# Optimization experiments

Measured on AMD Instinct MI355X. Metric: run time of the kernel, lower is better.

Reference implementation:

```python
import jax, jax.numpy as jnp
import numpy as np

NUM_HEADS = 16


def _local_attn(q, k, v, bias, nq, nk):
    """Blocked local attention, faithful to rearrange_to_dense_trunk semantics.
    q,k,v: [B,H,N,D]; bias: [B,Hb,N,N] (Hb broadcasts against H).
    Trunk i (queries [i*nq,(i+1)*nq)) attends keys at original indices
    [i*nq - pad_left, i*nq - pad_left + nk); out-of-range keys/values/bias are
    zero-padded (the module pads with zeros, no -inf key masking).
    Assumes N % nq == 0 (q_pad_length == 0, so the query mask loop is a no-op).
    """
    B, H, N, D = q.shape
    T = N // nq                      # n_trunks
    pad_left = (nk - nq) // 2
    Lp = (T - 1) * nq + nk           # padded key length so every window is full
    pad_right = Lp - pad_left - N
    k_p = jnp.pad(k, ((0, 0), (0, 0), (pad_left, pad_right), (0, 0)))
    v_p = jnp.pad(v, ((0, 0), (0, 0), (pad_left, pad_right), (0, 0)))
    b_p = jnp.pad(bias, ((0, 0), (0, 0), (0, 0), (pad_left, pad_right)))
    # window gather indices: [T, nk]
    kidx = jnp.arange(T)[:, None] * nq + jnp.arange(nk)[None, :]
    k_t = k_p[:, :, kidx, :]         # [B,H,T,nk,D]
    v_t = v_p[:, :, kidx, :]         # [B,H,T,nk,D]
    Bb, Hb = bias.shape[0], bias.shape[1]
    b_r = b_p.reshape(Bb, Hb, T, nq, Lp)
    b_t = jnp.take_along_axis(b_r, kidx[None, None, :, None, :], axis=-1)  # [Bb,Hb,T,nq,nk]
    q_t = q.reshape(B, H, T, nq, D)
    scores = jnp.einsum('bhtqd,bhtkd->bhtqk', q_t, k_t) + b_t
    w = jax.nn.softmax(scores, axis=-1)
    o = jnp.einsum('bhtqk,bhtkd->bhtqd', w, v_t)
    return o.reshape(B, H, N, D)


def setup_inputs() -> dict:
    key = jax.random.key(0)
    ks = jax.random.split(key, 8)
    B, N, C = 1, 4096, 256
    H, D = NUM_HEADS, 64
    HD = H * D
    q_x = jax.random.normal(ks[0], (B, N, C), dtype=jnp.float32)
    kv_x = jax.random.normal(ks[1], (B, N, C), dtype=jnp.float32)
    attn_bias = jax.random.normal(ks[2], (B, 1, N, N), dtype=jnp.float32) * 0.1
    Wq = jax.random.normal(ks[3], (C, HD), dtype=jnp.float32) / np.sqrt(C).astype(np.float32)
    Wk = jax.random.normal(ks[4], (C, HD), dtype=jnp.float32) / np.sqrt(C).astype(np.float32)
    Wv = jax.random.normal(ks[5], (C, HD), dtype=jnp.float32) / np.sqrt(C).astype(np.float32)
    Wg = jax.random.normal(ks[6], (C, HD), dtype=jnp.float32) / np.sqrt(C).astype(np.float32)
    Wo = jax.random.normal(ks[7], (HD, C), dtype=jnp.float32) / np.sqrt(HD).astype(np.float32)
    return {"q_x": q_x, "kv_x": kv_x, "attn_bias": attn_bias,
            "Wq": Wq, "Wk": Wk, "Wv": Wv, "Wg": Wg, "Wo": Wo,
            "n_queries": 64, "n_keys": 256}


def reference(q_x, kv_x, attn_bias, Wq, Wk, Wv, Wg, Wo, n_queries, n_keys):
    B, N, C = q_x.shape
    H = NUM_HEADS
    D = Wq.shape[-1] // H
    def split_heads(x):
        return x.reshape(B, N, H, D).transpose(0, 2, 1, 3)  # [B,H,N,D]
    q = split_heads(q_x @ Wq) / jnp.sqrt(jnp.float32(D))
    k = split_heads(kv_x @ Wk)
    v = split_heads(kv_x @ Wv)
    o = _local_attn(q, k, v, attn_bias, n_queries, n_keys)
    o = o.transpose(0, 2, 1, 3).reshape(B, N, H * D)
    g = jax.nn.sigmoid(q_x @ Wg)  # gating head
    return (o * g) @ Wo
```

## Files before the change

kernel.cpp:

```cpp
#include <hip/hip_runtime.h>

#define N_ 4096
#define C_ 256
#define H_ 16
#define D_ 64
#define HD_ 1024

typedef __attribute__((ext_vector_type(8))) __bf16 bf16x8;
typedef __attribute__((ext_vector_type(4))) __bf16 bf16x4;
typedef __attribute__((ext_vector_type(8))) _Float16 f16x8;
typedef __attribute__((ext_vector_type(4))) float f32x4;

__device__ __forceinline__ void gload16(const void* g, void* l) {
    __builtin_amdgcn_global_load_lds(
        (const __attribute__((address_space(1))) unsigned int*)g,
        (__attribute__((address_space(3))) unsigned int*)l, 16, 0, 0);
}

struct bf2 { __bf16 h, l; };
__device__ __forceinline__ bf2 split_bf16(float v) {
    bf2 r;
    r.h = (__bf16)v;
    r.l = (__bf16)(v - (float)r.h);
    return r;
}

__global__ __launch_bounds__(256) void convert_kernel(
    const float* __restrict__ q_x, const float* __restrict__ kv_x,
    const float* __restrict__ Wq, const float* __restrict__ Wk,
    const float* __restrict__ Wv, const float* __restrict__ Wg,
    const float* __restrict__ Wo,
    __bf16* __restrict__ Xh, __bf16* __restrict__ Xl,
    __bf16* __restrict__ WTh, __bf16* __restrict__ WTl,
    __bf16* __restrict__ WoTh, __bf16* __restrict__ WoTl)
{
    __shared__ float ts[64][65];
    const int b = blockIdx.x;
    const int tid = threadIdx.x;

    if (b < 512) {
        const int seg = b >> 8;
        const float* src = seg ? kv_x : q_x;
        __bf16* dh = Xh + (size_t)seg * 1048576;
        __bf16* dl = Xl + (size_t)seg * 1048576;
        const int base = (b & 255) * 4096 + tid * 16;
#pragma unroll
        for (int q = 0; q < 4; ++q) {
            float4 v = *(const float4*)&src[base + q * 4];
            bf16x4 hv, lv;
            bf2 s0 = split_bf16(v.x); hv[0] = s0.h; lv[0] = s0.l;
            bf2 s1 = split_bf16(v.y); hv[1] = s1.h; lv[1] = s1.l;
            bf2 s2 = split_bf16(v.z); hv[2] = s2.h; lv[2] = s2.l;
            bf2 s3 = split_bf16(v.w); hv[3] = s3.h; lv[3] = s3.l;
            *(bf16x4*)&dh[base + q * 4] = hv;
            *(bf16x4*)&dl[base + q * 4] = lv;
        }
        return;
    }

    const float* src;
    __bf16 *dh, *dl;
    int srcC, dstC, r0, c0;
    if (b < 768) {
        const int widx = (b - 512) >> 6;
        const int tile = (b - 512) & 63;
        src = (widx == 0) ? Wq : (widx == 1) ? Wk : (widx == 2) ? Wv : Wg;
        dh = WTh + (size_t)widx * 262144;
        dl = WTl + (size_t)widx * 262144;
        srcC = 1024; dstC = 256;
        r0 = (tile >> 4) * 64;
        c0 = (tile & 15) * 64;
    } else {
        const int tile = b - 768;
        src = Wo; dh = WoTh; dl = WoTl;
        srcC = 256; dstC = 1024;
        r0 = (tile >> 2) * 64;
        c0 = (tile & 3) * 64;
    }
    {
        const int r = tid >> 2;
        const int cch = (tid & 3) * 16;
#pragma unroll
        for (int q = 0; q < 4; ++q) {
            float4 v = *(const float4*)&src[(size_t)(r0 + r) * srcC + c0 + cch + q * 4];
            ts[r][cch + q * 4 + 0] = v.x;
            ts[r][cch + q * 4 + 1] = v.y;
            ts[r][cch + q * 4 + 2] = v.z;
            ts[r][cch + q * 4 + 3] = v.w;
        }
    }
    __syncthreads();
    {
        const int c = tid >> 2;
        const int rch = (tid & 3) * 16;
#pragma unroll
        for (int q = 0; q < 4; ++q) {
            bf16x4 hv, lv;
#pragma unroll
            for (int j = 0; j < 4; ++j) {
                bf2 s = split_bf16(ts[rch + q * 4 + j][c]);
                hv[j] = s.h; lv[j] = s.l;
            }
            *(bf16x4*)&dh[(size_t)(c0 + c) * dstC + r0 + rch + q * 4] = hv;
            *(bf16x4*)&dl[(size_t)(c0 + c) * dstC + r0 + rch + q * 4] = lv;
        }
    }
}

__global__ __launch_bounds__(256) void proj_mfma(
    const __bf16* __restrict__ Xh, const __bf16* __restrict__ Xl,
    const __bf16* __restrict__ WTh, const __bf16* __restrict__ WTl,
    _Float16* __restrict__ qh, _Float16* __restrict__ kh,
    _Float16* __restrict__ vh, _Float16* __restrict__ gh)
{
    __shared__ __align__(16) __bf16 smem[4 * 4096];
    __bf16* As_h = smem;
    __bf16* As_l = smem + 4096;
    __bf16* Bs_h = smem + 8192;
    __bf16* Bs_l = smem + 12288;

    const int bid  = blockIdx.x;
    const int g    = bid >> 8;
    const int tile = bid & 255;
    const int m0   = (tile >> 3) * 128;
    const int c0   = (tile & 7) * 128;

    const size_t xoff = (g == 1 || g == 2) ? 1048576 : 0;
    const __bf16* Ah = Xh + xoff;
    const __bf16* Al = Xl + xoff;
    const __bf16* Bh = WTh + (size_t)g * 262144;
    const __bf16* Bl = WTl + (size_t)g * 262144;

    const int tid  = threadIdx.x;
    const int wave = tid >> 6;
    const int lane = tid & 63;
    const int wr   = wave >> 1;
    const int wc   = wave & 1;

    const int srow = tid >> 2;
    const int selem = (tid & 3) * 8;
    const int sbyte = tid * 16;

    f32x4 acc[4][4];
#pragma unroll
    for (int i = 0; i < 4; ++i)
#pragma unroll
        for (int j = 0; j < 4; ++j) acc[i][j] = (f32x4){0.f, 0.f, 0.f, 0.f};

    const int frow = lane & 15;
    const int fk   = (lane >> 4) * 8;

    for (int kt = 0; kt < 256; kt += 32) {
        __syncthreads();
#pragma unroll
        for (int p = 0; p < 2; ++p) {
            const int r = srow + p * 64;
            gload16(Ah + (size_t)(m0 + r) * 256 + kt + selem, (char*)As_h + p * 4096 + sbyte);
            gload16(Al + (size_t)(m0 + r) * 256 + kt + selem, (char*)As_l + p * 4096 + sbyte);
            gload16(Bh + (size_t)(c0 + r) * 256 + kt + selem, (char*)Bs_h + p * 4096 + sbyte);
            gload16(Bl + (size_t)(c0 + r) * 256 + kt + selem, (char*)Bs_l + p * 4096 + sbyte);
        }
        __syncthreads();

        bf16x8 afh[4], afl[4], bfh[4], bfl[4];
#pragma unroll
        for (int f = 0; f < 4; ++f) {
            const int ar = (wr * 64 + f * 16 + frow) * 32 + fk;
            const int br = (wc * 64 + f * 16 + frow) * 32 + fk;
            afh[f] = *(const bf16x8*)&As_h[ar];
            afl[f] = *(const bf16x8*)&As_l[ar];
            bfh[f] = *(const bf16x8*)&Bs_h[br];
            bfl[f] = *(const bf16x8*)&Bs_l[br];
        }
#pragma unroll
        for (int i = 0; i < 4; ++i)
#pragma unroll
            for (int j = 0; j < 4; ++j) {
                acc[i][j] = __builtin_amdgcn_mfma_f32_16x16x32_bf16(afh[i], bfh[j], acc[i][j], 0, 0, 0);
                acc[i][j] = __builtin_amdgcn_mfma_f32_16x16x32_bf16(afl[i], bfh[j], acc[i][j], 0, 0, 0);
                acc[i][j] = __builtin_amdgcn_mfma_f32_16x16x32_bf16(afh[i], bfl[j], acc[i][j], 0, 0, 0);
            }
    }

    const int rbase = (lane >> 4) * 4;
    const int colc  = lane & 15;
    if (g == 3) {
#pragma unroll
        for (int i = 0; i < 4; ++i)
#pragma unroll
            for (int j = 0; j < 4; ++j) {
                const int c = c0 + wc * 64 + j * 16 + colc;
#pragma unroll
                for (int v = 0; v < 4; ++v) {
                    const int n = m0 + wr * 64 + i * 16 + rbase + v;
                    gh[(size_t)n * HD_ + c] = (_Float16)(1.f / (1.f + __expf(-acc[i][j][v])));
                }
            }
    } else {
        const float scale = (g == 0) ? 0.125f : 1.f;
        _Float16* dst = (g == 0) ? qh : (g == 1) ? kh : vh;
#pragma unroll
        for (int i = 0; i < 4; ++i)
#pragma unroll
            for (int j = 0; j < 4; ++j) {
                const int c = c0 + wc * 64 + j * 16 + colc;
                const int hh = c >> 6, dd = c & 63;
#pragma unroll
                for (int v = 0; v < 4; ++v) {
                    const int n = m0 + wr * 64 + i * 16 + rbase + v;
                    dst[((size_t)hh * N_ + n) * D_ + dd] = (_Float16)(acc[i][j][v] * scale);
                }
            }
    }
}

__global__ __launch_bounds__(256) void attn_mfma(
    const _Float16* __restrict__ qh, const _Float16* __restrict__ kh,
    const _Float16* __restrict__ vh, const float* __restrict__ bias,
    const _Float16* __restrict__ gh,
    __bf16* __restrict__ o_hi, __bf16* __restrict__ o_lo)
{
    __shared__ __align__(16) char smem[59392];
    _Float16* Qs = (_Float16*)smem;
    char* Ks = smem + 8192;
    _Float16* Vs = (_Float16*)(smem + 8192);
    _Float16* Ps = (_Float16*)(smem + 25600);

    const int bid = blockIdx.x;
    const int h = bid & 15;
    const int t = bid >> 4;
    const int tid = threadIdx.x;
    const int lane = tid & 63;
    const int wv = tid >> 6;
    const int frow = lane & 15;
    const int grp = lane >> 4;
    const int kbase = t * 64 - 96;

    const char* qbase = (const char*)qh + (size_t)(h * N_ + t * 64) * 128;
    const char* kbase_p = (const char*)kh + (size_t)h * N_ * 128;

#pragma unroll
    for (int q = 0; q < 2; ++q) {
        const int lin = q * 4096 + tid * 16;
        const int row = lin >> 7;
        const int ch = (lin >> 4) & 7;
        gload16(qbase + row * 128 + ((ch ^ (row & 7)) << 4), (char*)Qs + lin);
    }

    f32x4 sacc[16];

#pragma unroll
    for (int p = 0; p < 2; ++p) {
#pragma unroll
        for (int q = 0; q < 4; ++q) {
            const int lin = q * 4096 + tid * 16;
            const int row = lin >> 7;
            const int ch = (lin >> 4) & 7;
            const int kg = kbase + p * 128 + row;
            if ((unsigned)kg < (unsigned)N_) {
                gload16(kbase_p + (size_t)kg * 128 + ((ch ^ (row & 7)) << 4), Ks + lin);
            } else {
                *(float4*)(Ks + lin) = make_float4(0.f, 0.f, 0.f, 0.f);
            }
        }
        {
            const int rowg = t * 64 + wv * 16 + grp * 4;
#pragma unroll
            for (int j = 0; j < 8; ++j) {
                const int colg = kbase + p * 128 + j * 16 + frow;
                const bool ok = (unsigned)colg < (unsigned)N_;
#pragma unroll
                for (int v = 0; v < 4; ++v)
                    sacc[p * 8 + j][v] = ok ? bias[(size_t)(rowg + v) * N_ + colg] : 0.f;
            }
        }
        __syncthreads();
        const int rq = wv * 16 + frow;
#pragma unroll
        for (int ks = 0; ks < 2; ++ks) {
            const f16x8 aq = *(const f16x8*)((char*)Qs + rq * 128 + (((ks * 4 + grp) ^ (rq & 7)) << 4));
#pragma unroll
            for (int j = 0; j < 8; ++j) {
                const int rk = j * 16 + frow;
                const f16x8 bk = *(const f16x8*)(Ks + rk * 128 + (((ks * 4 + grp) ^ (rk & 7)) << 4));
                sacc[p * 8 + j] = __builtin_amdgcn_mfma_f32_16x16x32_f16(aq, bk, sacc[p * 8 + j], 0, 0, 0);
            }
        }
        __syncthreads();
    }

    float inv[4];
#pragma unroll
    for (int v = 0; v < 4; ++v) {
        float m = sacc[0][v];
#pragma unroll
        for (int f = 1; f < 16; ++f) m = fmaxf(m, sacc[f][v]);
        m = fmaxf(m, __shfl_xor(m, 1));
        m = fmaxf(m, __shfl_xor(m, 2));
        m = fmaxf(m, __shfl_xor(m, 4));
        m = fmaxf(m, __shfl_xor(m, 8));
        float l = 0.f;
#pragma unroll
        for (int f = 0; f < 16; ++f) {
            float e = __expf(sacc[f][v] - m);
            sacc[f][v] = e;
            l += e;
        }
        l += __shfl_xor(l, 1);
        l += __shfl_xor(l, 2);
        l += __shfl_xor(l, 4);
        l += __shfl_xor(l, 8);
        inv[v] = 1.f / l;
    }

    {
        const int rb = wv * 16 + grp * 4;
#pragma unroll
        for (int f = 0; f < 16; ++f) {
            const int col = (f >> 3) * 128 + (f & 7) * 16 + frow;
#pragma unroll
            for (int v = 0; v < 4; ++v)
                Ps[(rb + v) * 264 + col] = (_Float16)sacc[f][v];
        }
    }

    f32x4 oacc[4];
#pragma unroll
    for (int jd = 0; jd < 4; ++jd) oacc[jd] = (f32x4){0.f, 0.f, 0.f, 0.f};

#pragma unroll
    for (int c = 0; c < 2; ++c) {
        {
            const int sl = tid >> 1;
            const int d0 = (tid & 1) * 32;
            const int kg = kbase + c * 128 + sl;
            f16x8 vv[4];
            if ((unsigned)kg < (unsigned)N_) {
                const f16x8* vp = (const f16x8*)(vh + ((size_t)h * N_ + kg) * D_ + d0);
#pragma unroll
                for (int q = 0; q < 4; ++q) vv[q] = vp[q];
            } else {
#pragma unroll
                for (int q = 0; q < 4; ++q)
#pragma unroll
                    for (int e = 0; e < 8; ++e) vv[q][e] = (_Float16)0.f;
            }
#pragma unroll
            for (int q = 0; q < 4; ++q)
#pragma unroll
                for (int e = 0; e < 8; ++e)
                    Vs[(d0 + q * 8 + e) * 136 + sl] = vv[q][e];
        }
        __syncthreads();
        const int rp = wv * 16 + frow;
#pragma unroll
        for (int ks = 0; ks < 4; ++ks) {
            const f16x8 ap = *(const f16x8*)((char*)Ps + rp * 528 + c * 256 + ks * 64 + grp * 16);
#pragma unroll
            for (int jd = 0; jd < 4; ++jd) {
                const f16x8 bv = *(const f16x8*)((char*)Vs + (jd * 16 + frow) * 272 + ks * 64 + grp * 16);
                oacc[jd] = __builtin_amdgcn_mfma_f32_16x16x32_f16(ap, bv, oacc[jd], 0, 0, 0);
            }
        }
        __syncthreads();
    }

#pragma unroll
    for (int jd = 0; jd < 4; ++jd) {
        const int dcol = jd * 16 + frow;
        const int cg = h * 64 + dcol;
#pragma unroll
        for (int v = 0; v < 4; ++v) {
            const int n = t * 64 + wv * 16 + grp * 4 + v;
            const float gt = (float)gh[(size_t)n * HD_ + cg];
            const float val = oacc[jd][v] * inv[v] * gt;
            bf2 s = split_bf16(val);
            o_hi[(size_t)n * HD_ + cg] = s.h;
            o_lo[(size_t)n * HD_ + cg] = s.l;
        }
    }
}

__global__ __launch_bounds__(256) void out_mfma(
    const __bf16* __restrict__ o_hi, const __bf16* __restrict__ o_lo,
    const __bf16* __restrict__ WoTh, const __bf16* __restrict__ WoTl,
    float* __restrict__ out)
{
    __shared__ __align__(16) __bf16 smem[4 * 2048];
    __bf16* As_h = smem;
    __bf16* As_l = smem + 2048;
    __bf16* Bs_h = smem + 4096;
    __bf16* Bs_l = smem + 6144;

    const int bid = blockIdx.x;
    const int m0  = (bid >> 2) * 64;
    const int c0  = (bid & 3) * 64;

    const int tid  = threadIdx.x;
    const int wave = tid >> 6;
    const int lane = tid & 63;
    const int wr   = wave >> 1;
    const int wc   = wave & 1;

    const int srow  = tid >> 2;
    const int selem = (tid & 3) * 8;
    const int sbyte = tid * 16;

    f32x4 acc[2][2];
#pragma unroll
    for (int i = 0; i < 2; ++i)
#pragma unroll
        for (int j = 0; j < 2; ++j) acc[i][j] = (f32x4){0.f, 0.f, 0.f, 0.f};

    const int frow = lane & 15;
    const int fk   = (lane >> 4) * 8;

    for (int kt = 0; kt < 1024; kt += 32) {
        __syncthreads();
        gload16(o_hi + (size_t)(m0 + srow) * HD_ + kt + selem, (char*)As_h + sbyte);
        gload16(o_lo + (size_t)(m0 + srow) * HD_ + kt + selem, (char*)As_l + sbyte);
        gload16(WoTh + (size_t)(c0 + srow) * HD_ + kt + selem, (char*)Bs_h + sbyte);
        gload16(WoTl + (size_t)(c0 + srow) * HD_ + kt + selem, (char*)Bs_l + sbyte);
        __syncthreads();

        bf16x8 afh[2], afl[2], bfh[2], bfl[2];
#pragma unroll
        for (int f = 0; f < 2; ++f) {
            const int ar = (wr * 32 + f * 16 + frow) * 32 + fk;
            const int br = (wc * 32 + f * 16 + frow) * 32 + fk;
            afh[f] = *(const bf16x8*)&As_h[ar];
            afl[f] = *(const bf16x8*)&As_l[ar];
            bfh[f] = *(const bf16x8*)&Bs_h[br];
            bfl[f] = *(const bf16x8*)&Bs_l[br];
        }
#pragma unroll
        for (int i = 0; i < 2; ++i)
#pragma unroll
            for (int j = 0; j < 2; ++j) {
                acc[i][j] = __builtin_amdgcn_mfma_f32_16x16x32_bf16(afh[i], bfh[j], acc[i][j], 0, 0, 0);
                acc[i][j] = __builtin_amdgcn_mfma_f32_16x16x32_bf16(afl[i], bfh[j], acc[i][j], 0, 0, 0);
                acc[i][j] = __builtin_amdgcn_mfma_f32_16x16x32_bf16(afh[i], bfl[j], acc[i][j], 0, 0, 0);
            }
    }

    const int rbase = (lane >> 4) * 4;
    const int colc  = lane & 15;
#pragma unroll
    for (int i = 0; i < 2; ++i)
#pragma unroll
        for (int j = 0; j < 2; ++j) {
            const int c = c0 + wc * 32 + j * 16 + colc;
#pragma unroll
            for (int v = 0; v < 4; ++v) {
                const int n = m0 + wr * 32 + i * 16 + rbase + v;
                out[(size_t)n * C_ + c] = acc[i][j][v];
            }
        }
}

extern "C" void kernel_launch(void* const* d_in, const int* in_sizes, int n_in,
                              void* d_out, int out_size, void* d_ws, size_t ws_size,
                              hipStream_t stream)
{
    const float* q_x  = (const float*)d_in[0];
    const float* kv_x = (const float*)d_in[1];
    const float* bias = (const float*)d_in[2];
    const float* Wq   = (const float*)d_in[3];
    const float* Wk   = (const float*)d_in[4];
    const float* Wv   = (const float*)d_in[5];
    const float* Wg   = (const float*)d_in[6];
    const float* Wo   = (const float*)d_in[7];
    float* out = (float*)d_out;

    char* ws = (char*)d_ws;
    const size_t MB = 1048576;
    _Float16* qh  = (_Float16*)(ws);
    _Float16* kh  = (_Float16*)(ws + 8  * MB);
    _Float16* vh  = (_Float16*)(ws + 16 * MB);
    _Float16* gh  = (_Float16*)(ws + 24 * MB);
    __bf16* o_hi  = (__bf16*)(ws + 32 * MB);
    __bf16* o_lo  = (__bf16*)(ws + 40 * MB);
    __bf16* Xh    = (__bf16*)(ws + 48 * MB);
    __bf16* Xl    = (__bf16*)(ws + 52 * MB);
    __bf16* WTh   = (__bf16*)(ws + 56 * MB);
    __bf16* WTl   = (__bf16*)(ws + 58 * MB);
    __bf16* WoTh  = (__bf16*)(ws + 60 * MB);
    __bf16* WoTl  = (__bf16*)(ws + 60 * MB + 524288);

    convert_kernel<<<832, 256, 0, stream>>>(q_x, kv_x, Wq, Wk, Wv, Wg, Wo,
                                            Xh, Xl, WTh, WTl, WoTh, WoTl);
    proj_mfma<<<1024, 256, 0, stream>>>(Xh, Xl, WTh, WTl, qh, kh, vh, gh);
    attn_mfma<<<1024, 256, 0, stream>>>(qh, kh, vh, bias, gh, o_hi, o_lo);
    out_mfma<<<256, 256, 0, stream>>>(o_hi, o_lo, WoTh, WoTl, out);
}
```

Before: 196.0 us.

## Remap blocks per XCD for L2 locality and stage projection stores via LDS

Block indices in all three kernels are remapped so that blocks placed on the same XCD (blockIdx mod 8) work on related tiles: the same row groups for the GEMMs and consecutive trunks of one head for attention. The aim is better reuse in each XCD's L2 cache. The projection epilogue now writes results into a padded LDS tile, two passes of 64 rows each. It then issues 16-byte vectorized global stores instead of scattered 2-byte stores. The cost is extra barriers and LDS traffic in the epilogue, and the remap relies on the grid size being a multiple of 64.

New measurement: 196.9 us. About the same (+0.5%).

```diff
diff --git a/kernel.cpp b/kernel.cpp
--- a/kernel.cpp
+++ b/kernel.cpp
@@ -9,6 +9,7 @@
 typedef __attribute__((ext_vector_type(8))) __bf16 bf16x8;
 typedef __attribute__((ext_vector_type(4))) __bf16 bf16x4;
 typedef __attribute__((ext_vector_type(8))) _Float16 f16x8;
+typedef __attribute__((ext_vector_type(4))) _Float16 f16x4;
 typedef __attribute__((ext_vector_type(4))) float f32x4;
 
 __device__ __forceinline__ void gload16(const void* g, void* l) {
@@ -119,11 +120,13 @@
     __bf16* Bs_h = smem + 8192;
     __bf16* Bs_l = smem + 12288;
 
-    const int bid  = blockIdx.x;
-    const int g    = bid >> 8;
-    const int tile = bid & 255;
-    const int m0   = (tile >> 3) * 128;
-    const int c0   = (tile & 7) * 128;
+    const int lb  = blockIdx.x;
+    const int xcd = lb & 7;
+    const int idx = lb >> 3;
+    const int gr  = (idx >> 3) * 8 + xcd;
+    const int g   = gr >> 5;
+    const int m0  = (gr & 31) * 128;
+    const int c0  = (idx & 7) * 128;
 
     const size_t xoff = (g == 1 || g == 2) ? 1048576 : 0;
     const __bf16* Ah = Xh + xoff;
@@ -182,35 +185,50 @@
             }
     }
 
+    _Float16* Os = (_Float16*)smem;
     const int rbase = (lane >> 4) * 4;
     const int colc  = lane & 15;
-    if (g == 3) {
-#pragma unroll
-        for (int i = 0; i < 4; ++i)
-#pragma unroll
-            for (int j = 0; j < 4; ++j) {
-                const int c = c0 + wc * 64 + j * 16 + colc;
-#pragma unroll
-                for (int v = 0; v < 4; ++v) {
-                    const int n = m0 + wr * 64 + i * 16 + rbase + v;
-                    gh[(size_t)n * HD_ + c] = (_Float16)(1.f / (1.f + __expf(-acc[i][j][v])));
+    const float scale = (g == 0) ? 0.125f : 1.f;
+    const int er   = tid >> 2;
+    const int eseg = tid & 3;
+
+    for (int p = 0; p < 2; ++p) {
+        __syncthreads();
+        if (wr == p) {
+#pragma unroll
+            for (int i = 0; i < 4; ++i)
+#pragma unroll
+                for (int j = 0; j < 4; ++j) {
+                    const int rr = i * 16 + rbase;
+                    const int cc = wc * 64 + j * 16 + colc;
+#pragma unroll
+                    for (int v = 0; v < 4; ++v) {
+                        float x = acc[i][j][v];
+                        x = (g == 3) ? 1.f / (1.f + __expf(-x)) : x * scale;
+                        Os[(rr + v) * 132 + cc] = (_Float16)x;
+                    }
                 }
-            }
-    } else {
-        const float scale = (g == 0) ? 0.125f : 1.f;
-        _Float16* dst = (g == 0) ? qh : (g == 1) ? kh : vh;
-#pragma unroll
-        for (int i = 0; i < 4; ++i)
-#pragma unroll
-            for (int j = 0; j < 4; ++j) {
-                const int c = c0 + wc * 64 + j * 16 + colc;
-                const int hh = c >> 6, dd = c & 63;
-#pragma unroll
-                for (int v = 0; v < 4; ++v) {
-                    const int n = m0 + wr * 64 + i * 16 + rbase + v;
-                    dst[((size_t)hh * N_ + n) * D_ + dd] = (_Float16)(acc[i][j][v] * scale);
-                }
-            }
+        }
+        __syncthreads();
+        const int n = m0 + p * 64 + er;
+        __align__(16) _Float16 buf[32];
+#pragma unroll
+        for (int e = 0; e < 32; e += 4)
+            *(f16x4*)&buf[e] = *(const f16x4*)&Os[er * 132 + eseg * 32 + e];
+        if (g == 3) {
+            _Float16* dstp = gh + (size_t)n * HD_ + c0 + eseg * 32;
+#pragma unroll
+            for (int e = 0; e < 32; e += 8)
+                *(f16x8*)&dstp[e] = *(const f16x8*)&buf[e];
+        } else {
+            _Float16* dst = (g == 0) ? qh : (g == 1) ? kh : vh;
+            const int cglob = c0 + eseg * 32;
+            const int hh = cglob >> 6, dd = cglob & 63;
+            _Float16* dstp = dst + ((size_t)hh * N_ + n) * D_ + dd;
+#pragma unroll
+            for (int e = 0; e < 32; e += 8)
+                *(f16x8*)&dstp[e] = *(const f16x8*)&buf[e];
+        }
     }
 }
 
@@ -226,9 +244,11 @@
     _Float16* Vs = (_Float16*)(smem + 8192);
     _Float16* Ps = (_Float16*)(smem + 25600);
 
-    const int bid = blockIdx.x;
-    const int h = bid & 15;
-    const int t = bid >> 4;
+    const int lb  = blockIdx.x;
+    const int xcd = lb & 7;
+    const int j_  = lb >> 3;
+    const int h   = j_ >> 3;
+    const int t   = xcd * 8 + (j_ & 7);
     const int tid = threadIdx.x;
     const int lane = tid & 63;
     const int wv = tid >> 6;
@@ -392,9 +412,12 @@
     __bf16* Bs_h = smem + 4096;
     __bf16* Bs_l = smem + 6144;
 
-    const int bid = blockIdx.x;
-    const int m0  = (bid >> 2) * 64;
-    const int c0  = (bid & 3) * 64;
+    const int lb  = blockIdx.x;
+    const int xcd = lb & 7;
+    const int idx = lb >> 3;
+    const int rowg = (idx >> 2) * 8 + xcd;
+    const int m0  = rowg * 64;
+    const int c0  = (idx & 3) * 64;
 
     const int tid  = threadIdx.x;
     const int wave = tid >> 6;
```

## Use single fp16 MFMA for QKVG projection and remap blocks per XCD

Applied to the files above, without the earlier changes.

The input projection drops the split-bf16 three-MFMA scheme. Inputs and weights are converted once to fp16 and multiplied with one f16 MFMA per fragment, using a 64-wide K tile and an XOR-swizzled LDS layout. This cuts MFMA count, global traffic and conversion work at the cost of fp16 input precision. The proj, attention and output kernels also remap block IDs so that blocks sharing data land on the same XCD, aiming for better L2 reuse.

After: 173.3 us. 1.13x faster.

```diff
diff --git a/kernel.cpp b/kernel.cpp
--- a/kernel.cpp
+++ b/kernel.cpp
@@ -9,6 +9,7 @@
 typedef __attribute__((ext_vector_type(8))) __bf16 bf16x8;
 typedef __attribute__((ext_vector_type(4))) __bf16 bf16x4;
 typedef __attribute__((ext_vector_type(8))) _Float16 f16x8;
+typedef __attribute__((ext_vector_type(4))) _Float16 f16x4;
 typedef __attribute__((ext_vector_type(4))) float f32x4;
 
 __device__ __forceinline__ void gload16(const void* g, void* l) {
@@ -30,8 +31,7 @@
     const float* __restrict__ Wq, const float* __restrict__ Wk,
     const float* __restrict__ Wv, const float* __restrict__ Wg,
     const float* __restrict__ Wo,
-    __bf16* __restrict__ Xh, __bf16* __restrict__ Xl,
-    __bf16* __restrict__ WTh, __bf16* __restrict__ WTl,
+    _Float16* __restrict__ Xf, _Float16* __restrict__ WTf,
     __bf16* __restrict__ WoTh, __bf16* __restrict__ WoTl)
 {
     __shared__ float ts[64][65];
@@ -41,105 +41,115 @@
     if (b < 512) {
         const int seg = b >> 8;
         const float* src = seg ? kv_x : q_x;
-        __bf16* dh = Xh + (size_t)seg * 1048576;
-        __bf16* dl = Xl + (size_t)seg * 1048576;
+        _Float16* df = Xf + (size_t)seg * 1048576;
         const int base = (b & 255) * 4096 + tid * 16;
 #pragma unroll
         for (int q = 0; q < 4; ++q) {
             float4 v = *(const float4*)&src[base + q * 4];
-            bf16x4 hv, lv;
-            bf2 s0 = split_bf16(v.x); hv[0] = s0.h; lv[0] = s0.l;
-            bf2 s1 = split_bf16(v.y); hv[1] = s1.h; lv[1] = s1.l;
-            bf2 s2 = split_bf16(v.z); hv[2] = s2.h; lv[2] = s2.l;
-            bf2 s3 = split_bf16(v.w); hv[3] = s3.h; lv[3] = s3.l;
-            *(bf16x4*)&dh[base + q * 4] = hv;
-            *(bf16x4*)&dl[base + q * 4] = lv;
+            f16x4 fv;
+            fv[0] = (_Float16)v.x; fv[1] = (_Float16)v.y;
+            fv[2] = (_Float16)v.z; fv[3] = (_Float16)v.w;
+            *(f16x4*)&df[base + q * 4] = fv;
         }
         return;
     }
 
-    const float* src;
-    __bf16 *dh, *dl;
-    int srcC, dstC, r0, c0;
     if (b < 768) {
         const int widx = (b - 512) >> 6;
         const int tile = (b - 512) & 63;
-        src = (widx == 0) ? Wq : (widx == 1) ? Wk : (widx == 2) ? Wv : Wg;
-        dh = WTh + (size_t)widx * 262144;
-        dl = WTl + (size_t)widx * 262144;
-        srcC = 1024; dstC = 256;
-        r0 = (tile >> 4) * 64;
-        c0 = (tile & 15) * 64;
-    } else {
+        const float* src = (widx == 0) ? Wq : (widx == 1) ? Wk : (widx == 2) ? Wv : Wg;
+        _Float16* df = WTf + (size_t)widx * 262144;
+        const int r0 = (tile >> 4) * 64;
+        const int c0 = (tile & 15) * 64;
+        {
+            const int r = tid >> 2;
+            const int cch = (tid & 3) * 16;
+#pragma unroll
+            for (int q = 0; q < 4; ++q) {
+                float4 v = *(const float4*)&src[(size_t)(r0 + r) * 1024 + c0 + cch + q * 4];
+                ts[r][cch + q * 4 + 0] = v.x;
+                ts[r][cch + q * 4 + 1] = v.y;
+                ts[r][cch + q * 4 + 2] = v.z;
+                ts[r][cch + q * 4 + 3] = v.w;
+            }
+        }
+        __syncthreads();
+        {
+            const int c = tid >> 2;
+            const int rch = (tid & 3) * 16;
+#pragma unroll
+            for (int q = 0; q < 4; ++q) {
+                f16x4 fv;
+#pragma unroll
+                for (int j = 0; j < 4; ++j)
+                    fv[j] = (_Float16)ts[rch + q * 4 + j][c];
+                *(f16x4*)&df[(size_t)(c0 + c) * 256 + r0 + rch + q * 4] = fv;
+            }
+        }
+        return;
+    }
+
+    {
         const int tile = b - 768;
-        src = Wo; dh = WoTh; dl = WoTl;
-        srcC = 256; dstC = 1024;
-        r0 = (tile >> 2) * 64;
-        c0 = (tile & 3) * 64;
-    }
-    {
-        const int r = tid >> 2;
-        const int cch = (tid & 3) * 16;
-#pragma unroll
-        for (int q = 0; q < 4; ++q) {
-            float4 v = *(const float4*)&src[(size_t)(r0 + r) * srcC + c0 + cch + q * 4];
-            ts[r][cch + q * 4 + 0] = v.x;
-            ts[r][cch + q * 4 + 1] = v.y;
-            ts[r][cch + q * 4 + 2] = v.z;
-            ts[r][cch + q * 4 + 3] = v.w;
-        }
-    }
-    __syncthreads();
-    {
-        const int c = tid >> 2;
-        const int rch = (tid & 3) * 16;
-#pragma unroll
-        for (int q = 0; q < 4; ++q) {
-            bf16x4 hv, lv;
-#pragma unroll
-            for (int j = 0; j < 4; ++j) {
-                bf2 s = split_bf16(ts[rch + q * 4 + j][c]);
-                hv[j] = s.h; lv[j] = s.l;
-            }
-            *(bf16x4*)&dh[(size_t)(c0 + c) * dstC + r0 + rch + q * 4] = hv;
-            *(bf16x4*)&dl[(size_t)(c0 + c) * dstC + r0 + rch + q * 4] = lv;
+        const int r0 = (tile >> 2) * 64;
+        const int c0 = (tile & 3) * 64;
+        {
+            const int r = tid >> 2;
+            const int cch = (tid & 3) * 16;
+#pragma unroll
+            for (int q = 0; q < 4; ++q) {
+                float4 v = *(const float4*)&Wo[(size_t)(r0 + r) * 256 + c0 + cch + q * 4];
+                ts[r][cch + q * 4 + 0] = v.x;
+                ts[r][cch + q * 4 + 1] = v.y;
+                ts[r][cch + q * 4 + 2] = v.z;
+                ts[r][cch + q * 4 + 3] = v.w;
+            }
+        }
+        __syncthreads();
+        {
+            const int c = tid >> 2;
+            const int rch = (tid & 3) * 16;
+#pragma unroll
+            for (int q = 0; q < 4; ++q) {
+                bf16x4 hv, lv;
+#pragma unroll
+                for (int j = 0; j < 4; ++j) {
+                    bf2 s = split_bf16(ts[rch + q * 4 + j][c]);
+                    hv[j] = s.h; lv[j] = s.l;
+                }
+                *(bf16x4*)&WoTh[(size_t)(c0 + c) * 1024 + r0 + rch + q * 4] = hv;
+                *(bf16x4*)&WoTl[(size_t)(c0 + c) * 1024 + r0 + rch + q * 4] = lv;
+            }
         }
     }
 }
 
 __global__ __launch_bounds__(256) void proj_mfma(
-    const __bf16* __restrict__ Xh, const __bf16* __restrict__ Xl,
-    const __bf16* __restrict__ WTh, const __bf16* __restrict__ WTl,
+    const _Float16* __restrict__ Xf, const _Float16* __restrict__ WTf,
     _Float16* __restrict__ qh, _Float16* __restrict__ kh,
     _Float16* __restrict__ vh, _Float16* __restrict__ gh)
 {
-    __shared__ __align__(16) __bf16 smem[4 * 4096];
-    __bf16* As_h = smem;
-    __bf16* As_l = smem + 4096;
-    __bf16* Bs_h = smem + 8192;
-    __bf16* Bs_l = smem + 12288;
-
-    const int bid  = blockIdx.x;
-    const int g    = bid >> 8;
-    const int tile = bid & 255;
-    const int m0   = (tile >> 3) * 128;
-    const int c0   = (tile & 7) * 128;
-
-    const size_t xoff = (g == 1 || g == 2) ? 1048576 : 0;
-    const __bf16* Ah = Xh + xoff;
-    const __bf16* Al = Xl + xoff;
-    const __bf16* Bh = WTh + (size_t)g * 262144;
-    const __bf16* Bl = WTl + (size_t)g * 262144;
+    __shared__ __align__(16) _Float16 smem[2 * 8192];
+    _Float16* As = smem;
+    _Float16* Bs = smem + 8192;
+
+    const int lb  = blockIdx.x;
+    const int xcd = lb & 7;
+    const int gr  = (lb >> 6) * 8 + xcd;
+    const int g   = gr >> 5;
+    const int m0  = (gr & 31) * 128;
+    const int c0  = ((lb >> 3) & 7) * 128;
+
+    const _Float16* A = Xf + ((g == 1 || g == 2) ? 1048576 : 0);
+    const _Float16* B = WTf + (size_t)g * 262144;
 
     const int tid  = threadIdx.x;
     const int wave = tid >> 6;
     const int lane = tid & 63;
     const int wr   = wave >> 1;
     const int wc   = wave & 1;
-
-    const int srow = tid >> 2;
-    const int selem = (tid & 3) * 8;
-    const int sbyte = tid * 16;
+    const int frow = lane & 15;
+    const int grp  = lane >> 4;
 
     f32x4 acc[4][4];
 #pragma unroll
@@ -147,49 +157,45 @@
 #pragma unroll
         for (int j = 0; j < 4; ++j) acc[i][j] = (f32x4){0.f, 0.f, 0.f, 0.f};
 
-    const int frow = lane & 15;
-    const int fk   = (lane >> 4) * 8;
-
-    for (int kt = 0; kt < 256; kt += 32) {
-        __syncthreads();
-#pragma unroll
-        for (int p = 0; p < 2; ++p) {
-            const int r = srow + p * 64;
-            gload16(Ah + (size_t)(m0 + r) * 256 + kt + selem, (char*)As_h + p * 4096 + sbyte);
-            gload16(Al + (size_t)(m0 + r) * 256 + kt + selem, (char*)As_l + p * 4096 + sbyte);
-            gload16(Bh + (size_t)(c0 + r) * 256 + kt + selem, (char*)Bs_h + p * 4096 + sbyte);
-            gload16(Bl + (size_t)(c0 + r) * 256 + kt + selem, (char*)Bs_l + p * 4096 + sbyte);
-        }
-        __syncthreads();
-
-        bf16x8 afh[4], afl[4], bfh[4], bfl[4];
-#pragma unroll
-        for (int f = 0; f < 4; ++f) {
-            const int ar = (wr * 64 + f * 16 + frow) * 32 + fk;
-            const int br = (wc * 64 + f * 16 + frow) * 32 + fk;
-            afh[f] = *(const bf16x8*)&As_h[ar];
-            afl[f] = *(const bf16x8*)&As_l[ar];
-            bfh[f] = *(const bf16x8*)&Bs_h[br];
-            bfl[f] = *(const bf16x8*)&Bs_l[br];
-        }
+    const int srow = tid >> 3;
+    const int sch  = tid & 7;
+
+    for (int kt = 0; kt < 256; kt += 64) {
+        __syncthreads();
+#pragma unroll
+        for (int p = 0; p < 4; ++p) {
+            const int row = p * 32 + srow;
+            const int koff = kt + ((sch ^ (row & 7)) << 3);
+            gload16(A + (size_t)(m0 + row) * 256 + koff, (char*)As + p * 4096 + tid * 16);
+            gload16(B + (size_t)(c0 + row) * 256 + koff, (char*)Bs + p * 4096 + tid * 16);
+        }
+        __syncthreads();
+
+#pragma unroll
+        for (int ks = 0; ks < 2; ++ks) {
+            f16x8 af[4], bf[4];
+#pragma unroll
+            for (int f = 0; f < 4; ++f) {
+                const int ra = wr * 64 + f * 16 + frow;
+                const int rb = wc * 64 + f * 16 + frow;
+                af[f] = *(const f16x8*)((char*)As + ra * 128 + (((ks * 4 + grp) ^ (ra & 7)) << 4));
+                bf[f] = *(const f16x8*)((char*)Bs + rb * 128 + (((ks * 4 + grp) ^ (rb & 7)) << 4));
+            }
+#pragma unroll
+            for (int i = 0; i < 4; ++i)
+#pragma unroll
+                for (int j = 0; j < 4; ++j)
+                    acc[i][j] = __builtin_amdgcn_mfma_f32_16x16x32_f16(af[i], bf[j], acc[i][j], 0, 0, 0);
+        }
+    }
+
+    const int rbase = grp * 4;
+    if (g == 3) {
 #pragma unroll
         for (int i = 0; i < 4; ++i)
 #pragma unroll
             for (int j = 0; j < 4; ++j) {
-                acc[i][j] = __builtin_amdgcn_mfma_f32_16x16x32_bf16(afh[i], bfh[j], acc[i][j], 0, 0, 0);
-                acc[i][j] = __builtin_amdgcn_mfma_f32_16x16x32_bf16(afl[i], bfh[j], acc[i][j], 0, 0, 0);
-                acc[i][j] = __builtin_amdgcn_mfma_f32_16x16x32_bf16(afh[i], bfl[j], acc[i][j], 0, 0, 0);
-            }
-    }
-
-    const int rbase = (lane >> 4) * 4;
-    const int colc  = lane & 15;
-    if (g == 3) {
-#pragma unroll
-        for (int i = 0; i < 4; ++i)
-#pragma unroll
-            for (int j = 0; j < 4; ++j) {
-                const int c = c0 + wc * 64 + j * 16 + colc;
+                const int c = c0 + wc * 64 + j * 16 + frow;
 #pragma unroll
                 for (int v = 0; v < 4; ++v) {
                     const int n = m0 + wr * 64 + i * 16 + rbase + v;
@@ -203,7 +209,7 @@
         for (int i = 0; i < 4; ++i)
 #pragma unroll
             for (int j = 0; j < 4; ++j) {
-                const int c = c0 + wc * 64 + j * 16 + colc;
+                const int c = c0 + wc * 64 + j * 16 + frow;
                 const int hh = c >> 6, dd = c & 63;
 #pragma unroll
                 for (int v = 0; v < 4; ++v) {
@@ -226,9 +232,11 @@
     _Float16* Vs = (_Float16*)(smem + 8192);
     _Float16* Ps = (_Float16*)(smem + 25600);
 
-    const int bid = blockIdx.x;
-    const int h = bid & 15;
-    const int t = bid >> 4;
+    const int lb  = blockIdx.x;
+    const int xcd = lb & 7;
+    const int j_  = lb >> 3;
+    const int h   = j_ >> 3;
+    const int t   = xcd * 8 + (j_ & 7);
     const int tid = threadIdx.x;
     const int lane = tid & 63;
     const int wv = tid >> 6;
@@ -392,9 +400,12 @@
     __bf16* Bs_h = smem + 4096;
     __bf16* Bs_l = smem + 6144;
 
-    const int bid = blockIdx.x;
-    const int m0  = (bid >> 2) * 64;
-    const int c0  = (bid & 3) * 64;
+    const int lb  = blockIdx.x;
+    const int xcd = lb & 7;
+    const int idx = lb >> 3;
+    const int rowg = (idx >> 2) * 8 + xcd;
+    const int m0  = rowg * 64;
+    const int c0  = (idx & 3) * 64;
 
     const int tid  = threadIdx.x;
     const int wave = tid >> 6;
@@ -480,16 +491,14 @@
     _Float16* gh  = (_Float16*)(ws + 24 * MB);
     __bf16* o_hi  = (__bf16*)(ws + 32 * MB);
     __bf16* o_lo  = (__bf16*)(ws + 40 * MB);
-    __bf16* Xh    = (__bf16*)(ws + 48 * MB);
-    __bf16* Xl    = (__bf16*)(ws + 52 * MB);
-    __bf16* WTh   = (__bf16*)(ws + 56 * MB);
-    __bf16* WTl   = (__bf16*)(ws + 58 * MB);
-    __bf16* WoTh  = (__bf16*)(ws + 60 * MB);
-    __bf16* WoTl  = (__bf16*)(ws + 60 * MB + 524288);
+    _Float16* Xf  = (_Float16*)(ws + 48 * MB);
+    _Float16* WTf = (_Float16*)(ws + 52 * MB);
+    __bf16* WoTh  = (__bf16*)(ws + 54 * MB);
+    __bf16* WoTl  = (__bf16*)(ws + 54 * MB + 524288);
 
     convert_kernel<<<832, 256, 0, stream>>>(q_x, kv_x, Wq, Wk, Wv, Wg, Wo,
-                                            Xh, Xl, WTh, WTl, WoTh, WoTl);
-    proj_mfma<<<1024, 256, 0, stream>>>(Xh, Xl, WTh, WTl, qh, kh, vh, gh);
+                                            Xf, WTf, WoTh, WoTl);
+    proj_mfma<<<1024, 256, 0, stream>>>(Xf, WTf, qh, kh, vh, gh);
     attn_mfma<<<1024, 256, 0, stream>>>(qh, kh, vh, bias, gh, o_hi, o_lo);
     out_mfma<<<256, 256, 0, stream>>>(o_hi, o_lo, WoTh, WoTl, out);
 }
```
